# Optimization experiments

Measured on AMD Instinct MI355X. Metric: run time of the kernel, lower is better.

Reference implementation:

```python
import jax, jax.numpy as jnp
import numpy as np

NUM_HEADS = 8
WS = 7          # window size (hardcoded in source)
SR = 4          # sr_ratio
EPS = 1e-5


def _win_partition(t, ws, H, W):
    # t: [B, h, N, d] -> [B*h*nW, ws*ws, d]
    B, h, N, d = t.shape
    t = t.reshape(B * h, H // ws, ws, W // ws, ws, d)
    t = t.transpose(0, 1, 3, 2, 4, 5)
    return t.reshape(-1, ws * ws, d)


def _win_reverse(w, ws, H, W, h):
    # w: [B*h*nW, ws*ws, d] -> [B, H*W, h*d]
    d = w.shape[-1]
    Bh = w.shape[0] // ((H // ws) * (W // ws))
    x = w.reshape(Bh, H // ws, W // ws, ws, ws, d).transpose(0, 1, 3, 2, 4, 5)
    x = x.reshape(Bh // h, h, H, W, d).transpose(0, 2, 3, 1, 4)
    return x.reshape(Bh // h, H * W, h * d)


def setup_inputs() -> dict:
    key = jax.random.key(0)
    B, H, W, C = 32, 56, 56, 256
    N = H * W
    ks = jax.random.split(key, 10)
    s = lambda k, shp: jax.random.normal(k, shp, dtype=jnp.float32) * 0.02
    return {
        "x": jax.random.normal(ks[0], (B, N, C), dtype=jnp.float32),
        "lepe_lin_w": s(ks[1], (C, C)), "lepe_lin_b": jnp.zeros((C,), jnp.float32),
        "lepe_conv_w": s(ks[2], (3, 3, 1, C)), "lepe_conv_b": jnp.zeros((C,), jnp.float32),
        "sr_w": s(ks[3], (SR, SR, C, C)), "sr_b": jnp.zeros((C,), jnp.float32),
        "norm_g": jnp.ones((C,), jnp.float32), "norm_b": jnp.zeros((C,), jnp.float32),
        "q1_w": s(ks[4], (C, C // 2)), "kv1_w": s(ks[5], (C, C)),
        "q2_w": s(ks[6], (C, C // 2)), "kv2_w": s(ks[7], (C, C)),
        "proj_w": s(ks[8], (C, C)), "proj_b": jnp.zeros((C,), jnp.float32),
        "H": H, "W": W,
    }


def reference(x, lepe_lin_w, lepe_lin_b, lepe_conv_w, lepe_conv_b, sr_w, sr_b,
              norm_g, norm_b, q1_w, kv1_w, q2_w, kv2_w, proj_w, proj_b, H, W):
    B, N, C = x.shape
    h2 = NUM_HEADS // 2
    d = C // NUM_HEADS
    scale = d ** (-0.5)

    # lepe: linear -> depthwise 3x3 conv (NHWC) -> flatten back
    lep = (x @ lepe_lin_w + lepe_lin_b).reshape(B, H, W, C)
    lep = jax.lax.conv_general_dilated(
        lep, lepe_conv_w, window_strides=(1, 1), padding='SAME',
        dimension_numbers=('NHWC', 'HWIO', 'NHWC'), feature_group_count=C) + lepe_conv_b
    lepe = lep.reshape(B, N, C)

    # --- branch 1: global attention over sr-downsampled kv ---
    q1 = (x @ q1_w).reshape(B, N, h2, d).transpose(0, 2, 1, 3)         # [B,h2,N,d]
    img = x.reshape(B, H, W, C)
    x1_ = jax.lax.conv_general_dilated(
        img, sr_w, window_strides=(SR, SR), padding='VALID',
        dimension_numbers=('NHWC', 'HWIO', 'NHWC')) + sr_b              # [B,H/sr,W/sr,C]
    x1_ = x1_.reshape(B, -1, C)                                         # [B,N1,C]
    mu = jnp.mean(x1_, axis=-1, keepdims=True)
    var = jnp.mean(jnp.square(x1_ - mu), axis=-1, keepdims=True)
    x1_ = (x1_ - mu) * jax.lax.rsqrt(var + EPS) * norm_g + norm_b
    x1_ = jax.nn.gelu(x1_, approximate=False)
    kv1 = (x1_ @ kv1_w).reshape(B, -1, 2, h2, d).transpose(2, 0, 3, 1, 4)
    k1, v1 = kv1[0], kv1[1]                                             # [B,h2,N1,d]
    attn1 = jax.nn.softmax(jnp.einsum('bhnd,bhmd->bhnm', q1, k1) * scale, axis=-1)
    x1 = jnp.einsum('bhnm,bhmd->bhnd', attn1, v1)
    x1 = x1.transpose(0, 2, 1, 3).reshape(B, N, C // 2)

    # --- branch 2: 7x7 window attention ---
    q2 = (x @ q2_w).reshape(B, N, h2, d).transpose(0, 2, 1, 3)          # [B,h2,N,d]
    kv2 = (x @ kv2_w).reshape(B, -1, 2, h2, d).transpose(2, 0, 3, 1, 4)
    k2, v2 = kv2[0], kv2[1]
    q2w = _win_partition(q2, WS, H, W)                                  # [B*h2*nW,49,d]
    k2w = _win_partition(k2, WS, H, W)
    v2w = _win_partition(v2, WS, H, W)
    attn2 = jax.nn.softmax(jnp.einsum('wnd,wmd->wnm', q2w, k2w) * scale, axis=-1)
    x2w = jnp.einsum('wnm,wmd->wnd', attn2, v2w)
    x2 = _win_reverse(x2w, WS, H, W, h2)                                # [B,N,C/2]

    out = jnp.concatenate([x1, x2], axis=-1)
    out = (out + lepe) @ proj_w + proj_b
    return out
```

## Files before the change

kernel.cpp:

```cpp
#include <hip/hip_runtime.h>
#include <hip/hip_bf16.h>

typedef __hip_bfloat16 bf16;
typedef __attribute__((ext_vector_type(8))) short short8;
typedef __attribute__((ext_vector_type(4))) float floatx4;

__device__ __forceinline__ float toF(bf16 v){ return __bfloat162float(v); }
__device__ __forceinline__ float b2f(unsigned short u){
  return __uint_as_float(((unsigned int)u) << 16);
}
__device__ __forceinline__ unsigned short f2bu(float f){
  bf16 h = __float2bfloat16(f);
  return *(unsigned short*)&h;
}
__device__ __forceinline__ void storeT(bf16* p, float v){ *p = __float2bfloat16(v); }
__device__ __forceinline__ void storeT(float* p, float v){ *p = v; }

__global__ __launch_bounds__(256) void cvt_x_kernel(
    const float* __restrict__ in, bf16* __restrict__ out) {
  size_t i4 = ((size_t)blockIdx.x * 256 + threadIdx.x) * 4;
  float4 v = *(const float4*)(in + i4);
  ushort4 o;
  o.x = f2bu(v.x); o.y = f2bu(v.y); o.z = f2bu(v.z); o.w = f2bu(v.w);
  *(ushort4*)(out + i4) = o;
}

__global__ __launch_bounds__(256) void cvt_tr_kernel(
    const float* __restrict__ src, bf16* __restrict__ dst, int K, int N) {
  int idx = blockIdx.x * 256 + threadIdx.x;
  int k = idx / N, n = idx - k * N;
  dst[(size_t)n * K + k] = __float2bfloat16(src[idx]);
}

__global__ __launch_bounds__(256) void srbase_kernel(int* __restrict__ base) {
  int t = blockIdx.x * 256 + threadIdx.x;
  if (t >= 6272) return;
  int b = t / 196, p = t - b * 196;
  int oy = p / 14, ox = p - oy * 14;
  base[t] = ((b * 56 + oy * 4) * 56 + ox * 4) * 256;
}

template<typename OT>
__global__ __launch_bounds__(256) void gemm_mfma(
    const bf16* __restrict__ A, const bf16* __restrict__ BT,
    const float* __restrict__ bias, OT* __restrict__ C,
    int M, int K, int N) {
  __shared__ uint4 As[128 * 5];
  __shared__ uint4 Bs[128 * 5];
  const int tid = threadIdx.x;
  const int m0 = blockIdx.y * 128;
  const int n0 = blockIdx.x * 128;
  const int wave = tid >> 6, lane = tid & 63;
  const int wm = (wave >> 1) * 64, wn = (wave & 1) * 64;
  const int l15 = lane & 15, quad = lane >> 4;
  floatx4 zero = {0.f, 0.f, 0.f, 0.f};
  floatx4 acc[4][4];
#pragma unroll
  for (int i = 0; i < 4; i++)
#pragma unroll
    for (int j = 0; j < 4; j++) acc[i][j] = zero;

  for (int k0 = 0; k0 < K; k0 += 32) {
#pragma unroll
    for (int it = 0; it < 2; it++) {
      int id = it * 256 + tid;
      int row = id >> 2, seg = id & 3;
      As[row * 5 + seg] = *(const uint4*)(A + (size_t)(m0 + row) * K + k0 + seg * 8);
      Bs[row * 5 + seg] = *(const uint4*)(BT + (size_t)(n0 + row) * K + k0 + seg * 8);
    }
    __syncthreads();
    short8 af[4], bfr[4];
#pragma unroll
    for (int i = 0; i < 4; i++)
      af[i] = *(const short8*)&As[(wm + i * 16 + l15) * 5 + quad];
#pragma unroll
    for (int j = 0; j < 4; j++)
      bfr[j] = *(const short8*)&Bs[(wn + j * 16 + l15) * 5 + quad];
#pragma unroll
    for (int i = 0; i < 4; i++)
#pragma unroll
      for (int j = 0; j < 4; j++)
        acc[i][j] = __builtin_amdgcn_mfma_f32_16x16x32_bf16(af[i], bfr[j], acc[i][j], 0, 0, 0);
    __syncthreads();
  }
#pragma unroll
  for (int j = 0; j < 4; j++) {
    int n = n0 + wn + j * 16 + l15;
    float bv = bias ? bias[n] : 0.0f;
#pragma unroll
    for (int i = 0; i < 4; i++) {
      int m = m0 + wm + i * 16 + quad * 4;
#pragma unroll
      for (int r = 0; r < 4; r++)
        storeT(&C[(size_t)(m + r) * N + n], acc[i][j][r] + bv);
    }
  }
}

__global__ __launch_bounds__(256) void gemm_x3(
    const bf16* __restrict__ A, const bf16* __restrict__ BT,
    const float* __restrict__ lepe_b,
    bf16* __restrict__ L1, bf16* __restrict__ KV2, bf16* __restrict__ Q12) {
  __shared__ uint4 As[128 * 5];
  __shared__ uint4 Bs[128 * 5];
  const int sw = (blockIdx.x & 7) * 588 + (blockIdx.x >> 3);
  const int bx = sw % 6, by = sw / 6;
  const int m0 = by * 128;
  const int n0 = bx * 128;
  const int tid = threadIdx.x;
  const int wave = tid >> 6, lane = tid & 63;
  const int wm = (wave >> 1) * 64, wn = (wave & 1) * 64;
  const int l15 = lane & 15, quad = lane >> 4;
  floatx4 zero = {0.f, 0.f, 0.f, 0.f};
  floatx4 acc[4][4];
#pragma unroll
  for (int i = 0; i < 4; i++)
#pragma unroll
    for (int j = 0; j < 4; j++) acc[i][j] = zero;

  for (int k0 = 0; k0 < 256; k0 += 32) {
#pragma unroll
    for (int it = 0; it < 2; it++) {
      int id = it * 256 + tid;
      int row = id >> 2, seg = id & 3;
      As[row * 5 + seg] = *(const uint4*)(A + (size_t)(m0 + row) * 256 + k0 + seg * 8);
      Bs[row * 5 + seg] = *(const uint4*)(BT + (size_t)(n0 + row) * 256 + k0 + seg * 8);
    }
    __syncthreads();
    short8 af[4], bfr[4];
#pragma unroll
    for (int i = 0; i < 4; i++)
      af[i] = *(const short8*)&As[(wm + i * 16 + l15) * 5 + quad];
#pragma unroll
    for (int j = 0; j < 4; j++)
      bfr[j] = *(const short8*)&Bs[(wn + j * 16 + l15) * 5 + quad];
#pragma unroll
    for (int i = 0; i < 4; i++)
#pragma unroll
      for (int j = 0; j < 4; j++)
        acc[i][j] = __builtin_amdgcn_mfma_f32_16x16x32_bf16(af[i], bfr[j], acc[i][j], 0, 0, 0);
    __syncthreads();
  }
  const int segN = n0 >> 8;
  bf16* Cd = (segN == 0) ? L1 : (segN == 1) ? KV2 : Q12;
  const int nc0 = n0 & 255;
#pragma unroll
  for (int j = 0; j < 4; j++) {
    int nl = nc0 + wn + j * 16 + l15;
    float bv = (segN == 0) ? lepe_b[nl] : 0.0f;
#pragma unroll
    for (int i = 0; i < 4; i++) {
      int m = m0 + wm + i * 16 + quad * 4;
#pragma unroll
      for (int r = 0; r < 4; r++)
        Cd[(size_t)(m + r) * 256 + nl] = __float2bfloat16(acc[i][j][r] + bv);
    }
  }
}

__global__ __launch_bounds__(256) void gemm_sr(
    const bf16* __restrict__ X, const bf16* __restrict__ BT,
    const int* __restrict__ base, float* __restrict__ C) {
  __shared__ uint4 As[128 * 5];
  __shared__ uint4 Bs[128 * 5];
  __shared__ int sBase[128];
  const int tid = threadIdx.x;
  const int m0 = blockIdx.y * 128;
  const int n0 = blockIdx.x * 128;
  const int kz = blockIdx.z;
  if (tid < 128) sBase[tid] = base[m0 + tid];
  const int wave = tid >> 6, lane = tid & 63;
  const int wm = (wave >> 1) * 64, wn = (wave & 1) * 64;
  const int l15 = lane & 15, quad = lane >> 4;
  floatx4 zero = {0.f, 0.f, 0.f, 0.f};
  floatx4 acc[4][4];
#pragma unroll
  for (int i = 0; i < 4; i++)
#pragma unroll
    for (int j = 0; j < 4; j++) acc[i][j] = zero;
  __syncthreads();

  const int kbeg = kz * 512;
  for (int k0 = kbeg; k0 < kbeg + 512; k0 += 32) {
#pragma unroll
    for (int it = 0; it < 2; it++) {
      int id = it * 256 + tid;
      int row = id >> 2, seg = id & 3;
      int k = k0 + seg * 8;
      int kp = k >> 8, c = k & 255;
      int off = ((kp >> 2) * 56 + (kp & 3)) * 256 + c;
      As[row * 5 + seg] = *(const uint4*)(X + (size_t)sBase[row] + off);
      Bs[row * 5 + seg] = *(const uint4*)(BT + (size_t)(n0 + row) * 4096 + k);
    }
    __syncthreads();
    short8 af[4], bfr[4];
#pragma unroll
    for (int i = 0; i < 4; i++)
      af[i] = *(const short8*)&As[(wm + i * 16 + l15) * 5 + quad];
#pragma unroll
    for (int j = 0; j < 4; j++)
      bfr[j] = *(const short8*)&Bs[(wn + j * 16 + l15) * 5 + quad];
#pragma unroll
    for (int i = 0; i < 4; i++)
#pragma unroll
      for (int j = 0; j < 4; j++)
        acc[i][j] = __builtin_amdgcn_mfma_f32_16x16x32_bf16(af[i], bfr[j], acc[i][j], 0, 0, 0);
    __syncthreads();
  }
  float* Cp = C + (size_t)kz * (6272 * 256);
#pragma unroll
  for (int j = 0; j < 4; j++) {
    int n = n0 + wn + j * 16 + l15;
#pragma unroll
    for (int i = 0; i < 4; i++) {
      int m = m0 + wm + i * 16 + quad * 4;
#pragma unroll
      for (int r = 0; r < 4; r++)
        Cp[(size_t)(m + r) * 256 + n] = acc[i][j][r];
    }
  }
}

__global__ __launch_bounds__(256) void gemm_proj_mfma(
    const bf16* __restrict__ X1, const bf16* __restrict__ X2,
    const bf16* __restrict__ L2, const bf16* __restrict__ BT,
    const float* __restrict__ bias, float* __restrict__ C) {
  __shared__ uint4 As[128 * 5];
  __shared__ uint4 Bs[128 * 5];
  const int sw = (blockIdx.x & 7) * 196 + (blockIdx.x >> 3);
  const int tid = threadIdx.x;
  const int m0 = (sw >> 1) * 128;
  const int n0 = (sw & 1) * 128;
  const int wave = tid >> 6, lane = tid & 63;
  const int wm = (wave >> 1) * 64, wn = (wave & 1) * 64;
  const int l15 = lane & 15, quad = lane >> 4;
  floatx4 zero = {0.f, 0.f, 0.f, 0.f};
  floatx4 acc[4][4];
#pragma unroll
  for (int i = 0; i < 4; i++)
#pragma unroll
    for (int j = 0; j < 4; j++) acc[i][j] = zero;

  for (int k0 = 0; k0 < 256; k0 += 32) {
#pragma unroll
    for (int it = 0; it < 2; it++) {
      int id = it * 256 + tid;
      int row = id >> 2, seg = id & 3;
      int k = k0 + seg * 8;
      int mrow = m0 + row;
      const bf16* src = (k < 128) ? X1 + (size_t)mrow * 128 + k
                                  : X2 + (size_t)mrow * 128 + (k - 128);
      uint4 va = *(const uint4*)src;
      uint4 vl = *(const uint4*)(L2 + (size_t)mrow * 256 + k);
      const unsigned short* pa = (const unsigned short*)&va;
      const unsigned short* pl = (const unsigned short*)&vl;
      unsigned short ov[8];
#pragma unroll
      for (int e = 0; e < 8; e++) ov[e] = f2bu(b2f(pa[e]) + b2f(pl[e]));
      As[row * 5 + seg] = *(const uint4*)ov;
      Bs[row * 5 + seg] = *(const uint4*)(BT + (size_t)(n0 + row) * 256 + k);
    }
    __syncthreads();
    short8 af[4], bfr[4];
#pragma unroll
    for (int i = 0; i < 4; i++)
      af[i] = *(const short8*)&As[(wm + i * 16 + l15) * 5 + quad];
#pragma unroll
    for (int j = 0; j < 4; j++)
      bfr[j] = *(const short8*)&Bs[(wn + j * 16 + l15) * 5 + quad];
#pragma unroll
    for (int i = 0; i < 4; i++)
#pragma unroll
      for (int j = 0; j < 4; j++)
        acc[i][j] = __builtin_amdgcn_mfma_f32_16x16x32_bf16(af[i], bfr[j], acc[i][j], 0, 0, 0);
    __syncthreads();
  }
#pragma unroll
  for (int j = 0; j < 4; j++) {
    int n = n0 + wn + j * 16 + l15;
    float bv = bias[n];
#pragma unroll
    for (int i = 0; i < 4; i++) {
      int m = m0 + wm + i * 16 + quad * 4;
#pragma unroll
      for (int r = 0; r < 4; r++)
        C[(size_t)(m + r) * 256 + n] = acc[i][j][r] + bv;
    }
  }
}

__global__ __launch_bounds__(256) void dwconv8_kernel(
    const bf16* __restrict__ in, const float* __restrict__ w,
    const float* __restrict__ bias, bf16* __restrict__ out) {
  const int idx = blockIdx.x * 256 + threadIdx.x;
  const int c8 = (idx & 31) * 8;
  const int sp = idx >> 5;
  const int xx = sp % 56;
  const int yb = sp / 56;
  const int yy = yb % 56;
  const int b  = yb / 56;
  float4 bb0 = *(const float4*)&bias[c8];
  float4 bb1 = *(const float4*)&bias[c8 + 4];
  float acc[8] = {bb0.x, bb0.y, bb0.z, bb0.w, bb1.x, bb1.y, bb1.z, bb1.w};
#pragma unroll
  for (int dy = 0; dy < 3; dy++) {
    int y = yy + dy - 1;
    if ((unsigned)y >= 56u) continue;
#pragma unroll
    for (int dx = 0; dx < 3; dx++) {
      int x = xx + dx - 1;
      if ((unsigned)x >= 56u) continue;
      uint4 v = *(const uint4*)&in[((size_t)((b * 56 + y) * 56 + x)) * 256 + c8];
      const unsigned short* pv = (const unsigned short*)&v;
      float4 w0 = *(const float4*)&w[(dy * 3 + dx) * 256 + c8];
      float4 w1 = *(const float4*)&w[(dy * 3 + dx) * 256 + c8 + 4];
      float wf[8] = {w0.x, w0.y, w0.z, w0.w, w1.x, w1.y, w1.z, w1.w};
#pragma unroll
      for (int e = 0; e < 8; e++) acc[e] += b2f(pv[e]) * wf[e];
    }
  }
  unsigned short o[8];
#pragma unroll
  for (int e = 0; e < 8; e++) o[e] = f2bu(acc[e]);
  *(uint4*)&out[(size_t)sp * 256 + c8] = *(const uint4*)o;
}

__global__ __launch_bounds__(256) void ln_gelu_kernel(
    const float* __restrict__ in, const float* __restrict__ srb,
    const float* __restrict__ g, const float* __restrict__ bb,
    bf16* __restrict__ out) {
  const int tok = blockIdx.x;
  const int tid = threadIdx.x;
  float v = srb[tid];
  const float* p = in + (size_t)tok * 256 + tid;
#pragma unroll
  for (int c = 0; c < 8; c++) v += p[(size_t)c * 1605632];
  float s = v, s2 = v * v;
#pragma unroll
  for (int o = 32; o > 0; o >>= 1) {
    s += __shfl_down(s, o, 64);
    s2 += __shfl_down(s2, o, 64);
  }
  __shared__ float rs[4], rs2[4];
  int wid = tid >> 6, lane = tid & 63;
  if (lane == 0) { rs[wid] = s; rs2[wid] = s2; }
  __syncthreads();
  float tot = rs[0] + rs[1] + rs[2] + rs[3];
  float tot2 = rs2[0] + rs2[1] + rs2[2] + rs2[3];
  float mean = tot * (1.0f / 256.0f);
  float var = tot2 * (1.0f / 256.0f) - mean * mean;
  float y = (v - mean) * rsqrtf(var + 1e-5f) * g[tid] + bb[tid];
  out[(size_t)tok * 256 + tid] =
      __float2bfloat16(0.5f * y * (1.0f + erff(y * 0.70710678118654752f)));
}

__global__ __launch_bounds__(256) void attn1_mfma(
    const bf16* __restrict__ Q12, const float* __restrict__ KV,
    bf16* __restrict__ O) {
  __shared__ bf16 sk[224 * 32];
  __shared__ bf16 svT[32 * 232];
  __shared__ bf16 pbuf[4][64 * 32];
  const int b = blockIdx.z, h = blockIdx.y, chunk = blockIdx.x;
  const int tid = threadIdx.x;
  const int wave = tid >> 6, lane = tid & 63;
  const int l15 = lane & 15, quad = lane >> 4;
  for (int i = tid; i < 224 * 8; i += 256) {
    int m = i >> 3, c = i & 7;
    float4 kf = {0.f, 0.f, 0.f, 0.f}, vf = {0.f, 0.f, 0.f, 0.f};
    if (m < 196) {
      const float* p = KV + ((size_t)(b * 196 + m)) * 256 + h * 32 + c * 4;
      kf = *(const float4*)p;
      vf = *(const float4*)(p + 128);
    }
    ushort4 ko;
    ko.x = f2bu(kf.x); ko.y = f2bu(kf.y); ko.z = f2bu(kf.z); ko.w = f2bu(kf.w);
    *(ushort4*)&sk[m * 32 + c * 4] = ko;
    svT[(c * 4 + 0) * 232 + m] = __float2bfloat16(vf.x);
    svT[(c * 4 + 1) * 232 + m] = __float2bfloat16(vf.y);
    svT[(c * 4 + 2) * 232 + m] = __float2bfloat16(vf.z);
    svT[(c * 4 + 3) * 232 + m] = __float2bfloat16(vf.w);
  }
  __syncthreads();
  const int q0 = chunk * 256 + wave * 64;
  short8 aq[4];
#pragma unroll
  for (int i = 0; i < 4; i++) {
    int qr = q0 + i * 16 + l15; if (qr > 3135) qr = 3135;
    aq[i] = *(const short8*)(Q12 + ((size_t)(b * 3136 + qr)) * 256 + h * 32 + quad * 8);
  }
  const float scale = 0.17677669529663687f;
  floatx4 zero = {0.f, 0.f, 0.f, 0.f};
  floatx4 acc[4][2];
  float lsum[4][4];
#pragma unroll
  for (int i = 0; i < 4; i++) {
    acc[i][0] = zero; acc[i][1] = zero;
#pragma unroll
    for (int r = 0; r < 4; r++) lsum[i][r] = 0.f;
  }
  bf16* pw = pbuf[wave];
  for (int c = 0; c < 7; c++) {
    const int kv0 = c * 32;
    short8 bk[2];
#pragma unroll
    for (int n = 0; n < 2; n++)
      bk[n] = *(const short8*)&sk[(kv0 + n * 16 + l15) * 32 + quad * 8];
    floatx4 s[4][2];
#pragma unroll
    for (int i = 0; i < 4; i++)
#pragma unroll
      for (int n = 0; n < 2; n++)
        s[i][n] = __builtin_amdgcn_mfma_f32_16x16x32_bf16(aq[i], bk[n], zero, 0, 0, 0);
#pragma unroll
    for (int i = 0; i < 4; i++)
#pragma unroll
      for (int n = 0; n < 2; n++) {
        bool valid = (kv0 + n * 16 + l15) < 196;
#pragma unroll
        for (int r = 0; r < 4; r++) {
          float p = valid ? __expf(s[i][n][r] * scale) : 0.f;
          lsum[i][r] += p;
          pw[(i * 16 + quad * 4 + r) * 32 + n * 16 + l15] = __float2bfloat16(p);
        }
      }
    asm volatile("s_waitcnt lgkmcnt(0)" ::: "memory");
    short8 ap[4], bv[2];
#pragma unroll
    for (int i = 0; i < 4; i++)
      ap[i] = *(const short8*)&pw[(i * 16 + l15) * 32 + quad * 8];
#pragma unroll
    for (int n = 0; n < 2; n++)
      bv[n] = *(const short8*)&svT[(n * 16 + l15) * 232 + kv0 + quad * 8];
#pragma unroll
    for (int i = 0; i < 4; i++)
#pragma unroll
      for (int n = 0; n < 2; n++)
        acc[i][n] = __builtin_amdgcn_mfma_f32_16x16x32_bf16(ap[i], bv[n], acc[i][n], 0, 0, 0);
  }
#pragma unroll
  for (int i = 0; i < 4; i++)
#pragma unroll
    for (int r = 0; r < 4; r++) {
      float v = lsum[i][r];
      v += __shfl_xor(v, 1, 64);
      v += __shfl_xor(v, 2, 64);
      v += __shfl_xor(v, 4, 64);
      v += __shfl_xor(v, 8, 64);
      lsum[i][r] = 1.0f / v;
    }
#pragma unroll
  for (int i = 0; i < 4; i++)
#pragma unroll
    for (int r = 0; r < 4; r++) {
      int qr = q0 + i * 16 + quad * 4 + r;
      if (qr < 3136) {
        bf16* op = O + ((size_t)(b * 3136 + qr)) * 128 + h * 32;
        op[l15]      = __float2bfloat16(acc[i][0][r] * lsum[i][r]);
        op[16 + l15] = __float2bfloat16(acc[i][1][r] * lsum[i][r]);
      }
    }
}

__global__ __launch_bounds__(256) void attn2_mfma(
    const bf16* __restrict__ Q12, const bf16* __restrict__ KV2,
    bf16* __restrict__ O) {
  __shared__ bf16 sk[64 * 136];
  __shared__ bf16 pb[4][64 * 72];
  const int b = blockIdx.y;
  const int win = blockIdx.x;
  const int wy = win >> 3, wx = win & 7;
  const int tid = threadIdx.x;
  const int wave = tid >> 6, lane = tid & 63;
  const int l15 = lane & 15, quad = lane >> 4;
  const int h = wave;

  for (int i = tid; i < 49 * 16; i += 256) {
    int m = i >> 4, c = i & 15;
    int iy = m / 7, ix = m - iy * 7;
    int n = (wy * 7 + iy) * 56 + wx * 7 + ix;
    *(uint4*)&sk[m * 136 + c * 8] =
        *(const uint4*)&KV2[((size_t)(b * 3136 + n)) * 256 + c * 8];
  }

  short8 bvv[2][2];
#pragma unroll
  for (int ks = 0; ks < 2; ks++)
#pragma unroll
    for (int nt = 0; nt < 2; nt++)
#pragma unroll
      for (int e = 0; e < 8; e++) {
        int k = ks * 32 + quad * 8 + e; if (k > 48) k = 48;
        int iy = k / 7, ix = k - iy * 7;
        int n = (wy * 7 + iy) * 56 + wx * 7 + ix;
        bvv[ks][nt][e] = ((const short*)KV2)[((size_t)(b * 3136 + n)) * 256
                                             + 128 + h * 32 + nt * 16 + l15];
      }

  short8 aq[4];
#pragma unroll
  for (int i = 0; i < 4; i++) {
    int lq = i * 16 + l15; if (lq > 48) lq = 48;
    int iy = lq / 7, ix = lq - iy * 7;
    int n = (wy * 7 + iy) * 56 + wx * 7 + ix;
    aq[i] = *(const short8*)(Q12 + ((size_t)(b * 3136 + n)) * 256 + 128 + h * 32 + quad * 8);
  }
  __syncthreads();

  const float scale = 0.17677669529663687f;
  floatx4 zero = {0.f, 0.f, 0.f, 0.f};
  floatx4 acc[4][2];
  float lsum[4][4];
#pragma unroll
  for (int i = 0; i < 4; i++) {
    acc[i][0] = zero; acc[i][1] = zero;
#pragma unroll
    for (int r = 0; r < 4; r++) lsum[i][r] = 0.f;
  }
  bf16* pw = pb[wave];
#pragma unroll
  for (int c = 0; c < 2; c++) {
    const int kv0 = c * 32;
    short8 bk[2];
#pragma unroll
    for (int n = 0; n < 2; n++)
      bk[n] = *(const short8*)&sk[(kv0 + n * 16 + l15) * 136 + h * 32 + quad * 8];
    floatx4 s[4][2];
#pragma unroll
    for (int i = 0; i < 4; i++)
#pragma unroll
      for (int n = 0; n < 2; n++)
        s[i][n] = __builtin_amdgcn_mfma_f32_16x16x32_bf16(aq[i], bk[n], zero, 0, 0, 0);
#pragma unroll
    for (int i = 0; i < 4; i++)
#pragma unroll
      for (int n = 0; n < 2; n++) {
        bool valid = (kv0 + n * 16 + l15) < 49;
#pragma unroll
        for (int r = 0; r < 4; r++) {
          float p = valid ? __expf(s[i][n][r] * scale) : 0.f;
          lsum[i][r] += p;
          pw[(i * 16 + quad * 4 + r) * 72 + kv0 + n * 16 + l15] = __float2bfloat16(p);
        }
      }
  }
  asm volatile("s_waitcnt lgkmcnt(0)" ::: "memory");
#pragma unroll
  for (int ks = 0; ks < 2; ks++) {
    short8 ap[4];
#pragma unroll
    for (int i = 0; i < 4; i++)
      ap[i] = *(const short8*)&pw[(i * 16 + l15) * 72 + ks * 32 + quad * 8];
#pragma unroll
    for (int i = 0; i < 4; i++)
#pragma unroll
      for (int nt = 0; nt < 2; nt++)
        acc[i][nt] = __builtin_amdgcn_mfma_f32_16x16x32_bf16(ap[i], bvv[ks][nt], acc[i][nt], 0, 0, 0);
  }
#pragma unroll
  for (int i = 0; i < 4; i++)
#pragma unroll
    for (int r = 0; r < 4; r++) {
      float v = lsum[i][r];
      v += __shfl_xor(v, 1, 64);
      v += __shfl_xor(v, 2, 64);
      v += __shfl_xor(v, 4, 64);
      v += __shfl_xor(v, 8, 64);
      lsum[i][r] = 1.0f / v;
    }
#pragma unroll
  for (int i = 0; i < 4; i++)
#pragma unroll
    for (int r = 0; r < 4; r++) {
      int lq = i * 16 + quad * 4 + r;
      if (lq < 49) {
        int iy = lq / 7, ix = lq - iy * 7;
        int n = (wy * 7 + iy) * 56 + wx * 7 + ix;
        bf16* op = O + ((size_t)(b * 3136 + n)) * 128 + h * 32;
        op[l15]      = __float2bfloat16(acc[i][0][r] * lsum[i][r]);
        op[16 + l15] = __float2bfloat16(acc[i][1][r] * lsum[i][r]);
      }
    }
}

extern "C" void kernel_launch(void* const* d_in, const int* in_sizes, int n_in,
                              void* d_out, int out_size, void* d_ws, size_t ws_size,
                              hipStream_t stream) {
  const float* x           = (const float*)d_in[0];
  const float* lepe_lin_w  = (const float*)d_in[1];
  const float* lepe_lin_b  = (const float*)d_in[2];
  const float* lepe_conv_w = (const float*)d_in[3];
  const float* lepe_conv_b = (const float*)d_in[4];
  const float* sr_w        = (const float*)d_in[5];
  const float* sr_b        = (const float*)d_in[6];
  const float* norm_g      = (const float*)d_in[7];
  const float* norm_b      = (const float*)d_in[8];
  const float* q1_w        = (const float*)d_in[9];
  const float* kv1_w       = (const float*)d_in[10];
  const float* q2_w        = (const float*)d_in[11];
  const float* kv2_w       = (const float*)d_in[12];
  const float* proj_w      = (const float*)d_in[13];
  const float* proj_b      = (const float*)d_in[14];
  float* out = (float*)d_out;

  char* ws = (char*)d_ws;
  char* ob = (char*)d_out;
  const size_t szBNC = 100352ull * 256 * 2;
  const size_t szBNh = 100352ull * 128 * 2;
  bf16*  xb  = (bf16*)ob;
  bf16*  Q12 = (bf16*)(ob + szBNC);
  bf16*  L1  = (bf16*)ws;
  float* X1Ppart = (float*)ws;
  bf16*  X1N = (bf16*)ob;
  float* KV1 = (float*)(ob + 8388608);
  bf16*  X1  = (bf16*)ws;
  bf16*  L2  = (bf16*)(ws + szBNC);
  bf16*  X2  = (bf16*)(ws + 2 * szBNC);
  char*  wtb = ws + 2 * szBNC + szBNh;
  bf16* wT_x    = (bf16*)(wtb);
  bf16* wT_kv1  = (bf16*)(wtb + 393216);
  bf16* wT_proj = (bf16*)(wtb + 524288);
  bf16* wT_sr   = (bf16*)(wtb + 655360);
  int*  srbase  = (int*)(wtb + 655360 + 2097152);
  bf16* KV2     = (bf16*)(wtb + 655360 + 2097152 + 32768);

  cvt_x_kernel<<<25088, 256, 0, stream>>>(x, xb);
  cvt_tr_kernel<<<256, 256, 0, stream>>>(lepe_lin_w, wT_x, 256, 256);
  cvt_tr_kernel<<<256, 256, 0, stream>>>(kv2_w, wT_x + 256 * 256, 256, 256);
  cvt_tr_kernel<<<128, 256, 0, stream>>>(q1_w, wT_x + 512 * 256, 256, 128);
  cvt_tr_kernel<<<128, 256, 0, stream>>>(q2_w, wT_x + 640 * 256, 256, 128);
  cvt_tr_kernel<<<256, 256, 0, stream>>>(kv1_w, wT_kv1, 256, 256);
  cvt_tr_kernel<<<256, 256, 0, stream>>>(proj_w, wT_proj, 256, 256);
  cvt_tr_kernel<<<4096, 256, 0, stream>>>(sr_w, wT_sr, 4096, 256);
  srbase_kernel<<<25, 256, 0, stream>>>(srbase);

  gemm_x3<<<4704, 256, 0, stream>>>(xb, wT_x, lepe_lin_b, L1, KV2, Q12);

  dwconv8_kernel<<<12544, 256, 0, stream>>>(L1, lepe_conv_w, lepe_conv_b, L2);

  attn2_mfma<<<dim3(64, 32), 256, 0, stream>>>(Q12, KV2, X2);

  gemm_sr<<<dim3(2, 49, 8), 256, 0, stream>>>(xb, wT_sr, srbase, X1Ppart);
  ln_gelu_kernel<<<6272, 256, 0, stream>>>(X1Ppart, sr_b, norm_g, norm_b, X1N);
  gemm_mfma<float><<<dim3(2, 49), 256, 0, stream>>>(
      X1N, wT_kv1, nullptr, KV1, 6272, 256, 256);
  attn1_mfma<<<dim3(13, 4, 32), 256, 0, stream>>>(Q12, KV1, X1);

  gemm_proj_mfma<<<1568, 256, 0, stream>>>(
      X1, X2, L2, wT_proj, proj_b, out);
}
```

Baseline: 547.9 us.

## Use direct global-to-LDS loads in GEMMs and merge weight prep kernels

Replaces the register-staged global-to-shared tile loads in the GEMM kernels with the global_load_lds builtin, which writes 16-byte segments straight into LDS. The LDS layout changes from a padded 5-uint4 row stride to an unpadded 32-element row stride to match the per-wave contiguous writes. This removes VGPR staging and some instructions but may add LDS bank conflicts on the MFMA fragment reads. Separately, eight small weight-transpose and index kernels are merged into one prep launch to cut launch overhead.

```diff
diff --git a/kernel.cpp b/kernel.cpp
--- a/kernel.cpp
+++ b/kernel.cpp
@@ -15,6 +15,12 @@
 }
 __device__ __forceinline__ void storeT(bf16* p, float v){ *p = __float2bfloat16(v); }
 __device__ __forceinline__ void storeT(float* p, float v){ *p = v; }
+
+__device__ __forceinline__ void gl2l16(const void* g, void* l) {
+  __builtin_amdgcn_global_load_lds(
+      (const __attribute__((address_space(1))) unsigned int*)g,
+      (__attribute__((address_space(3))) unsigned int*)l, 16, 0, 0);
+}
 
 __global__ __launch_bounds__(256) void cvt_x_kernel(
     const float* __restrict__ in, bf16* __restrict__ out) {
@@ -25,19 +31,34 @@
   *(ushort4*)(out + i4) = o;
 }
 
-__global__ __launch_bounds__(256) void cvt_tr_kernel(
-    const float* __restrict__ src, bf16* __restrict__ dst, int K, int N) {
-  int idx = blockIdx.x * 256 + threadIdx.x;
+__global__ __launch_bounds__(256) void prep_kernel(
+    const float* __restrict__ sr_w, const float* __restrict__ lepe_w,
+    const float* __restrict__ kv2_w, const float* __restrict__ q1_w,
+    const float* __restrict__ q2_w, const float* __restrict__ kv1_w,
+    const float* __restrict__ proj_w,
+    bf16* __restrict__ wT_sr, bf16* __restrict__ wT_x,
+    bf16* __restrict__ wT_kv1, bf16* __restrict__ wT_proj,
+    int* __restrict__ srbase) {
+  const int bid = blockIdx.x, tid = threadIdx.x;
+  const float* src; bf16* dst; int K, N, idx;
+  if (bid < 4096)      { src = sr_w;   dst = wT_sr;          K = 4096; N = 256; idx = bid * 256 + tid; }
+  else if (bid < 4352) { src = lepe_w; dst = wT_x;           K = 256;  N = 256; idx = (bid - 4096) * 256 + tid; }
+  else if (bid < 4608) { src = kv2_w;  dst = wT_x + 65536;   K = 256;  N = 256; idx = (bid - 4352) * 256 + tid; }
+  else if (bid < 4736) { src = q1_w;   dst = wT_x + 131072;  K = 256;  N = 128; idx = (bid - 4608) * 256 + tid; }
+  else if (bid < 4864) { src = q2_w;   dst = wT_x + 163840;  K = 256;  N = 128; idx = (bid - 4736) * 256 + tid; }
+  else if (bid < 5120) { src = kv1_w;  dst = wT_kv1;         K = 256;  N = 256; idx = (bid - 4864) * 256 + tid; }
+  else if (bid < 5376) { src = proj_w; dst = wT_proj;        K = 256;  N = 256; idx = (bid - 5120) * 256 + tid; }
+  else {
+    int t = (bid - 5376) * 256 + tid;
+    if (t < 6272) {
+      int b = t / 196, p = t - b * 196;
+      int oy = p / 14, ox = p - oy * 14;
+      srbase[t] = ((b * 56 + oy * 4) * 56 + ox * 4) * 256;
+    }
+    return;
+  }
   int k = idx / N, n = idx - k * N;
   dst[(size_t)n * K + k] = __float2bfloat16(src[idx]);
-}
-
-__global__ __launch_bounds__(256) void srbase_kernel(int* __restrict__ base) {
-  int t = blockIdx.x * 256 + threadIdx.x;
-  if (t >= 6272) return;
-  int b = t / 196, p = t - b * 196;
-  int oy = p / 14, ox = p - oy * 14;
-  base[t] = ((b * 56 + oy * 4) * 56 + ox * 4) * 256;
 }
 
 template<typename OT>
@@ -45,14 +66,15 @@
     const bf16* __restrict__ A, const bf16* __restrict__ BT,
     const float* __restrict__ bias, OT* __restrict__ C,
     int M, int K, int N) {
-  __shared__ uint4 As[128 * 5];
-  __shared__ uint4 Bs[128 * 5];
+  __shared__ bf16 As[128 * 32];
+  __shared__ bf16 Bs[128 * 32];
   const int tid = threadIdx.x;
   const int m0 = blockIdx.y * 128;
   const int n0 = blockIdx.x * 128;
   const int wave = tid >> 6, lane = tid & 63;
   const int wm = (wave >> 1) * 64, wn = (wave & 1) * 64;
   const int l15 = lane & 15, quad = lane >> 4;
+  const int srow = lane >> 2, sseg = lane & 3;
   floatx4 zero = {0.f, 0.f, 0.f, 0.f};
   floatx4 acc[4][4];
 #pragma unroll
@@ -62,20 +84,20 @@
 
   for (int k0 = 0; k0 < K; k0 += 32) {
 #pragma unroll
-    for (int it = 0; it < 2; it++) {
-      int id = it * 256 + tid;
-      int row = id >> 2, seg = id & 3;
-      As[row * 5 + seg] = *(const uint4*)(A + (size_t)(m0 + row) * K + k0 + seg * 8);
-      Bs[row * 5 + seg] = *(const uint4*)(BT + (size_t)(n0 + row) * K + k0 + seg * 8);
+    for (int t = 0; t < 2; t++) {
+      int rb = wave * 32 + t * 16;
+      int r = rb + srow;
+      gl2l16(A + (size_t)(m0 + r) * K + k0 + sseg * 8, &As[rb * 32]);
+      gl2l16(BT + (size_t)(n0 + r) * K + k0 + sseg * 8, &Bs[rb * 32]);
     }
     __syncthreads();
     short8 af[4], bfr[4];
 #pragma unroll
     for (int i = 0; i < 4; i++)
-      af[i] = *(const short8*)&As[(wm + i * 16 + l15) * 5 + quad];
+      af[i] = *(const short8*)&As[(wm + i * 16 + l15) * 32 + quad * 8];
 #pragma unroll
     for (int j = 0; j < 4; j++)
-      bfr[j] = *(const short8*)&Bs[(wn + j * 16 + l15) * 5 + quad];
+      bfr[j] = *(const short8*)&Bs[(wn + j * 16 + l15) * 32 + quad * 8];
 #pragma unroll
     for (int i = 0; i < 4; i++)
 #pragma unroll
@@ -101,8 +123,8 @@
     const bf16* __restrict__ A, const bf16* __restrict__ BT,
     const float* __restrict__ lepe_b,
     bf16* __restrict__ L1, bf16* __restrict__ KV2, bf16* __restrict__ Q12) {
-  __shared__ uint4 As[128 * 5];
-  __shared__ uint4 Bs[128 * 5];
+  __shared__ bf16 As[128 * 32];
+  __shared__ bf16 Bs[128 * 32];
   const int sw = (blockIdx.x & 7) * 588 + (blockIdx.x >> 3);
   const int bx = sw % 6, by = sw / 6;
   const int m0 = by * 128;
@@ -111,6 +133,7 @@
   const int wave = tid >> 6, lane = tid & 63;
   const int wm = (wave >> 1) * 64, wn = (wave & 1) * 64;
   const int l15 = lane & 15, quad = lane >> 4;
+  const int srow = lane >> 2, sseg = lane & 3;
   floatx4 zero = {0.f, 0.f, 0.f, 0.f};
   floatx4 acc[4][4];
 #pragma unroll
@@ -120,20 +143,20 @@
 
   for (int k0 = 0; k0 < 256; k0 += 32) {
 #pragma unroll
-    for (int it = 0; it < 2; it++) {
-      int id = it * 256 + tid;
-      int row = id >> 2, seg = id & 3;
-      As[row * 5 + seg] = *(const uint4*)(A + (size_t)(m0 + row) * 256 + k0 + seg * 8);
-      Bs[row * 5 + seg] = *(const uint4*)(BT + (size_t)(n0 + row) * 256 + k0 + seg * 8);
+    for (int t = 0; t < 2; t++) {
+      int rb = wave * 32 + t * 16;
+      int r = rb + srow;
+      gl2l16(A + (size_t)(m0 + r) * 256 + k0 + sseg * 8, &As[rb * 32]);
+      gl2l16(BT + (size_t)(n0 + r) * 256 + k0 + sseg * 8, &Bs[rb * 32]);
     }
     __syncthreads();
     short8 af[4], bfr[4];
 #pragma unroll
     for (int i = 0; i < 4; i++)
-      af[i] = *(const short8*)&As[(wm + i * 16 + l15) * 5 + quad];
+      af[i] = *(const short8*)&As[(wm + i * 16 + l15) * 32 + quad * 8];
 #pragma unroll
     for (int j = 0; j < 4; j++)
-      bfr[j] = *(const short8*)&Bs[(wn + j * 16 + l15) * 5 + quad];
+      bfr[j] = *(const short8*)&Bs[(wn + j * 16 + l15) * 32 + quad * 8];
 #pragma unroll
     for (int i = 0; i < 4; i++)
 #pragma unroll
@@ -161,45 +184,44 @@
 __global__ __launch_bounds__(256) void gemm_sr(
     const bf16* __restrict__ X, const bf16* __restrict__ BT,
     const int* __restrict__ base, float* __restrict__ C) {
-  __shared__ uint4 As[128 * 5];
-  __shared__ uint4 Bs[128 * 5];
-  __shared__ int sBase[128];
+  __shared__ bf16 As[128 * 32];
+  __shared__ bf16 Bs[128 * 32];
   const int tid = threadIdx.x;
   const int m0 = blockIdx.y * 128;
   const int n0 = blockIdx.x * 128;
   const int kz = blockIdx.z;
-  if (tid < 128) sBase[tid] = base[m0 + tid];
   const int wave = tid >> 6, lane = tid & 63;
   const int wm = (wave >> 1) * 64, wn = (wave & 1) * 64;
   const int l15 = lane & 15, quad = lane >> 4;
+  const int srow = lane >> 2, sseg = lane & 3;
+  const int mb0 = base[m0 + wave * 32 + srow];
+  const int mb1 = base[m0 + wave * 32 + 16 + srow];
   floatx4 zero = {0.f, 0.f, 0.f, 0.f};
   floatx4 acc[4][4];
 #pragma unroll
   for (int i = 0; i < 4; i++)
 #pragma unroll
     for (int j = 0; j < 4; j++) acc[i][j] = zero;
-  __syncthreads();
 
   const int kbeg = kz * 512;
   for (int k0 = kbeg; k0 < kbeg + 512; k0 += 32) {
-#pragma unroll
-    for (int it = 0; it < 2; it++) {
-      int id = it * 256 + tid;
-      int row = id >> 2, seg = id & 3;
-      int k = k0 + seg * 8;
-      int kp = k >> 8, c = k & 255;
-      int off = ((kp >> 2) * 56 + (kp & 3)) * 256 + c;
-      As[row * 5 + seg] = *(const uint4*)(X + (size_t)sBase[row] + off);
-      Bs[row * 5 + seg] = *(const uint4*)(BT + (size_t)(n0 + row) * 4096 + k);
+    int k = k0 + sseg * 8;
+    int kp = k >> 8, c = k & 255;
+    int off = ((kp >> 2) * 56 + (kp & 3)) * 256 + c;
+#pragma unroll
+    for (int t = 0; t < 2; t++) {
+      int rb = wave * 32 + t * 16;
+      gl2l16(X + (size_t)(t ? mb1 : mb0) + off, &As[rb * 32]);
+      gl2l16(BT + (size_t)(n0 + rb + srow) * 4096 + k, &Bs[rb * 32]);
     }
     __syncthreads();
     short8 af[4], bfr[4];
 #pragma unroll
     for (int i = 0; i < 4; i++)
-      af[i] = *(const short8*)&As[(wm + i * 16 + l15) * 5 + quad];
+      af[i] = *(const short8*)&As[(wm + i * 16 + l15) * 32 + quad * 8];
 #pragma unroll
     for (int j = 0; j < 4; j++)
-      bfr[j] = *(const short8*)&Bs[(wn + j * 16 + l15) * 5 + quad];
+      bfr[j] = *(const short8*)&Bs[(wn + j * 16 + l15) * 32 + quad * 8];
 #pragma unroll
     for (int i = 0; i < 4; i++)
 #pragma unroll
@@ -226,7 +248,7 @@
     const bf16* __restrict__ L2, const bf16* __restrict__ BT,
     const float* __restrict__ bias, float* __restrict__ C) {
   __shared__ uint4 As[128 * 5];
-  __shared__ uint4 Bs[128 * 5];
+  __shared__ bf16 Bs[128 * 32];
   const int sw = (blockIdx.x & 7) * 196 + (blockIdx.x >> 3);
   const int tid = threadIdx.x;
   const int m0 = (sw >> 1) * 128;
@@ -234,6 +256,7 @@
   const int wave = tid >> 6, lane = tid & 63;
   const int wm = (wave >> 1) * 64, wn = (wave & 1) * 64;
   const int l15 = lane & 15, quad = lane >> 4;
+  const int srow = lane >> 2, sseg = lane & 3;
   floatx4 zero = {0.f, 0.f, 0.f, 0.f};
   floatx4 acc[4][4];
 #pragma unroll
@@ -242,6 +265,11 @@
     for (int j = 0; j < 4; j++) acc[i][j] = zero;
 
   for (int k0 = 0; k0 < 256; k0 += 32) {
+#pragma unroll
+    for (int t = 0; t < 2; t++) {
+      int rb = wave * 32 + t * 16;
+      gl2l16(BT + (size_t)(n0 + rb + srow) * 256 + k0 + sseg * 8, &Bs[rb * 32]);
+    }
 #pragma unroll
     for (int it = 0; it < 2; it++) {
       int id = it * 256 + tid;
@@ -258,7 +286,6 @@
 #pragma unroll
       for (int e = 0; e < 8; e++) ov[e] = f2bu(b2f(pa[e]) + b2f(pl[e]));
       As[row * 5 + seg] = *(const uint4*)ov;
-      Bs[row * 5 + seg] = *(const uint4*)(BT + (size_t)(n0 + row) * 256 + k);
     }
     __syncthreads();
     short8 af[4], bfr[4];
@@ -267,7 +294,7 @@
       af[i] = *(const short8*)&As[(wm + i * 16 + l15) * 5 + quad];
 #pragma unroll
     for (int j = 0; j < 4; j++)
-      bfr[j] = *(const short8*)&Bs[(wn + j * 16 + l15) * 5 + quad];
+      bfr[j] = *(const short8*)&Bs[(wn + j * 16 + l15) * 32 + quad * 8];
 #pragma unroll
     for (int i = 0; i < 4; i++)
 #pragma unroll
@@ -624,14 +651,9 @@
   bf16* KV2     = (bf16*)(wtb + 655360 + 2097152 + 32768);
 
   cvt_x_kernel<<<25088, 256, 0, stream>>>(x, xb);
-  cvt_tr_kernel<<<256, 256, 0, stream>>>(lepe_lin_w, wT_x, 256, 256);
-  cvt_tr_kernel<<<256, 256, 0, stream>>>(kv2_w, wT_x + 256 * 256, 256, 256);
-  cvt_tr_kernel<<<128, 256, 0, stream>>>(q1_w, wT_x + 512 * 256, 256, 128);
-  cvt_tr_kernel<<<128, 256, 0, stream>>>(q2_w, wT_x + 640 * 256, 256, 128);
-  cvt_tr_kernel<<<256, 256, 0, stream>>>(kv1_w, wT_kv1, 256, 256);
-  cvt_tr_kernel<<<256, 256, 0, stream>>>(proj_w, wT_proj, 256, 256);
-  cvt_tr_kernel<<<4096, 256, 0, stream>>>(sr_w, wT_sr, 4096, 256);
-  srbase_kernel<<<25, 256, 0, stream>>>(srbase);
+  prep_kernel<<<5401, 256, 0, stream>>>(
+      sr_w, lepe_lin_w, kv2_w, q1_w, q2_w, kv1_w, proj_w,
+      wT_sr, wT_x, wT_kv1, wT_proj, srbase);
 
   gemm_x3<<<4704, 256, 0, stream>>>(xb, wT_x, lepe_lin_b, L1, KV2, Q12);
 
```

New measurement: 536.6 us. 2.1% less time.
